# Optimization experiments

Measured on AMD Instinct MI355X. Metric: run time of the kernel, lower is better.

## Reference

```python
import jax, jax.numpy as jnp
import numpy as np

N_HEADS = 16
DIM = 1024
BS, SLEN = 2, 2048
EPS = 1e-12  # F.normalize eps


def setup_inputs() -> dict:
    key = jax.random.key(0)
    ks = jax.random.split(key, 10)
    d = DIM
    inp = {
        "x": jax.random.normal(ks[0], (BS, SLEN, d), dtype=jnp.float32),
        # causal attention mask, as produced by get_masks(causal=True)
        "mask": jnp.tril(jnp.ones((SLEN, SLEN), dtype=bool))[None].repeat(BS, axis=0),
        "Wq": jax.random.normal(ks[1], (d, d), dtype=jnp.float32) / np.sqrt(d),
        "bq": jax.random.normal(ks[2], (d,), dtype=jnp.float32) * 0.02,
        "Wk": jax.random.normal(ks[3], (d, d), dtype=jnp.float32) / np.sqrt(d),
        "bk": jax.random.normal(ks[4], (d,), dtype=jnp.float32) * 0.02,
        "Wv": jax.random.normal(ks[5], (d, d), dtype=jnp.float32) / np.sqrt(d),
        "bv": jax.random.normal(ks[6], (d,), dtype=jnp.float32) * 0.02,
        "Wo": jax.random.normal(ks[7], (d, d), dtype=jnp.float32) / np.sqrt(d),
        "bo": jax.random.normal(ks[8], (d,), dtype=jnp.float32) * 0.02,
        # learnable scale for normalized (cosine) attention
        "attention_scale": jnp.ones((1,), dtype=jnp.float32) / np.sqrt(d // N_HEADS),
    }
    return inp


def _shape(t, bs, h, dph):
    # (bs, len, dim) -> (bs, h, len, dph)
    return t.reshape(bs, -1, h, dph).transpose(0, 2, 1, 3)


def reference(x, mask, Wq, bq, Wk, bk, Wv, bv, Wo, bo, attention_scale):
    bs, qlen, dim = x.shape
    h = N_HEADS
    dph = dim // h

    q = _shape(x @ Wq + bq, bs, h, dph)  # (bs, h, qlen, dph)
    k = _shape(x @ Wk + bk, bs, h, dph)
    v = _shape(x @ Wv + bv, bs, h, dph)

    # normalized (cosine) attention: L2-normalize q and k, learned scale
    q = q / jnp.maximum(jnp.linalg.norm(q, axis=-1, keepdims=True), EPS)
    k = k / jnp.maximum(jnp.linalg.norm(k, axis=-1, keepdims=True), EPS)
    q = q * attention_scale

    scores = jnp.einsum("bhqd,bhkd->bhqk", q, k)  # (bs, h, qlen, klen)
    scores = jnp.where(mask[:, None, :, :], scores, -jnp.inf)
    weights = jax.nn.softmax(scores, axis=-1)

    ctx = jnp.einsum("bhqk,bhkd->bhqd", weights, v)
    ctx = ctx.transpose(0, 2, 1, 3).reshape(bs, qlen, dim)
    return ctx @ Wo + bo
```

## Files before the change

kernel.cpp:

```cpp
#include <hip/hip_runtime.h>
#include <math.h>

#define NH 16
#define DPH 64
#define SLEN 2048
#define BSZ 2
#define DIM 1024
#define NTOK (BSZ * SLEN)
#define LOG2E 1.44269504088896f

typedef unsigned short ushortT;
typedef __attribute__((ext_vector_type(8))) short short8;
typedef __attribute__((ext_vector_type(4))) short s16x4;
typedef __attribute__((ext_vector_type(4))) float f32x4;

typedef __attribute__((address_space(1))) const unsigned int gu32c;
typedef __attribute__((address_space(3))) unsigned int lu32;

__device__ __forceinline__ void gld16(const void* g, void* l) {
    __builtin_amdgcn_global_load_lds((gu32c*)g, (lu32*)l, 16, 0, 0);
}

__device__ __forceinline__ ushortT f2bf(float f) {
    unsigned int u = __builtin_bit_cast(unsigned int, f);
    u = u + 0x7fffu + ((u >> 16) & 1u);
    return (ushortT)(u >> 16);
}

__global__ __launch_bounds__(256) void cvt_all(const float* __restrict__ x,
                                               ushortT* __restrict__ xb,
                                               const float* __restrict__ W0, const float* __restrict__ W1,
                                               const float* __restrict__ W2, const float* __restrict__ W3,
                                               ushortT* __restrict__ T0, ushortT* __restrict__ T1,
                                               ushortT* __restrict__ T2, ushortT* __restrict__ T3) {
    __shared__ float tile[64][65];
    const int tid = threadIdx.x;
    const int bid = blockIdx.x;
    if (bid < 2048) {
        size_t i = (size_t)bid * 256 + tid;
        float4 a = *(const float4*)&x[i * 8];
        float4 b = *(const float4*)&x[i * 8 + 4];
        short8 v;
        v[0] = (short)f2bf(a.x); v[1] = (short)f2bf(a.y);
        v[2] = (short)f2bf(a.z); v[3] = (short)f2bf(a.w);
        v[4] = (short)f2bf(b.x); v[5] = (short)f2bf(b.y);
        v[6] = (short)f2bf(b.z); v[7] = (short)f2bf(b.w);
        *(short8*)&xb[i * 8] = v;
        return;
    }
    const int widx = bid - 2048;
    const int z = widx >> 8, rem = widx & 255;
    const float* W = z == 0 ? W0 : z == 1 ? W1 : z == 2 ? W2 : W3;
    ushortT* T = z == 0 ? T0 : z == 1 ? T1 : z == 2 ? T2 : T3;
    const int kb = (rem >> 4) * 64, nb = (rem & 15) * 64;
#pragma unroll
    for (int it = 0; it < 4; it++) {
        int chunk = it * 256 + tid;
        int r = chunk >> 4, c4 = (chunk & 15) * 4;
        *(float4*)&tile[r][c4] = *(const float4*)&W[(size_t)(kb + r) * DIM + nb + c4];
    }
    __syncthreads();
#pragma unroll
    for (int it = 0; it < 2; it++) {
        int chunk = it * 256 + tid;
        int n = chunk >> 3, k8 = (chunk & 7) * 8;
        short8 o;
#pragma unroll
        for (int j = 0; j < 8; j++) o[j] = (short)f2bf(tile[k8 + j][n]);
        *(short8*)&T[(size_t)(nb + n) * DIM + kb + k8] = o;
    }
}

__global__ __launch_bounds__(512, 2) void gemm_qkv8(const ushortT* __restrict__ A,
                                                    const ushortT* __restrict__ Bt,
                                                    const float* __restrict__ bq,
                                                    const float* __restrict__ bk,
                                                    const float* __restrict__ bv,
                                                    const float* __restrict__ ascale,
                                                    ushortT* __restrict__ Qb,
                                                    ushortT* __restrict__ Kb,
                                                    ushortT* __restrict__ VF) {
    __shared__ __align__(16) ushortT lds[65536];
    const int tid = threadIdx.x;
    const int lane = tid & 63, wid = tid >> 6;
    const int wm = wid >> 2, wn = wid & 3;
    const int lo = lane & 15, hi = lane >> 4;
    const int bid = blockIdx.x;
    const int swz = (bid & 7) * 24 + (bid >> 3);
    const int bx = swz % 12, by = swz / 12;
    const int row0 = by * 256, col0 = bx * 256;
    const int srow2 = tid >> 2, sc = tid & 3;
    f32x4 acc[8][4] = {};
    short8 af[4], bfr[4];

    auto stage = [&](int isA, int buf, int ksh, int kt) {
        const ushortT* g = isA ? A : Bt;
        int r0 = isA ? row0 : col0;
        int base = (isA ? 0 : 32768) + (buf * 2 + ksh) * 8192;
#pragma unroll
        for (int r = 0; r < 2; r++) {
            int rl = r * 128 + srow2;
            int gch = sc ^ ((rl >> 1) & 3);
            gld16(&g[(size_t)(r0 + rl) * DIM + kt * 64 + ksh * 32 + gch * 8],
                  &lds[base + r * 4096 + tid * 8]);
        }
    };
    auto loadA = [&](int buf, int ks, int mh) {
        int base = (buf * 2 + ks) * 8192;
#pragma unroll
        for (int mm = 0; mm < 4; mm++) {
            int row = wm * 128 + (mh * 4 + mm) * 16 + lo;
            af[mm] = *(const short8*)&lds[base + row * 32 + (hi ^ ((row >> 1) & 3)) * 8];
        }
    };
    auto loadB = [&](int buf, int ks) {
        int base = 32768 + (buf * 2 + ks) * 8192;
#pragma unroll
        for (int n = 0; n < 4; n++) {
            int row = wn * 64 + n * 16 + lo;
            bfr[n] = *(const short8*)&lds[base + row * 32 + (hi ^ ((row >> 1) & 3)) * 8];
        }
    };
    auto mfma16 = [&](int mh) {
        __builtin_amdgcn_s_setprio(1);
#pragma unroll
        for (int mm = 0; mm < 4; mm++)
#pragma unroll
            for (int n = 0; n < 4; n++)
                acc[mh * 4 + mm][n] = __builtin_amdgcn_mfma_f32_16x16x32_bf16(
                    af[mm], bfr[n], acc[mh * 4 + mm][n], 0, 0, 0);
        __builtin_amdgcn_s_setprio(0);
    };

    stage(1, 0, 0, 0); stage(0, 0, 0, 0);
    stage(1, 0, 1, 0); stage(0, 0, 1, 0);
    stage(1, 1, 0, 1); stage(0, 1, 0, 1);

#pragma unroll 1
    for (int it = 0; it < 8; ++it) {
        const int o = it * 2 + 1;
        const bool more = (it < 7);
        asm volatile("s_waitcnt vmcnt(8)" ::: "memory");
        asm volatile("s_barrier" ::: "memory");
        loadA(0, 0, 0); loadB(0, 0);
        stage(1, 1, 1, o);
        mfma16(0);
        asm volatile("s_barrier" ::: "memory");
        loadA(0, 0, 1);
        stage(0, 1, 1, o);
        mfma16(1);
        asm volatile("s_waitcnt vmcnt(8)" ::: "memory");
        asm volatile("s_barrier" ::: "memory");
        loadA(0, 1, 0); loadB(0, 1);
        if (more) stage(1, 0, 0, o + 1);
        mfma16(0);
        asm volatile("s_barrier" ::: "memory");
        loadA(0, 1, 1);
        if (more) stage(0, 0, 0, o + 1);
        mfma16(1);
        if (more) { asm volatile("s_waitcnt vmcnt(8)" ::: "memory"); }
        else      { asm volatile("s_waitcnt vmcnt(4)" ::: "memory"); }
        asm volatile("s_barrier" ::: "memory");
        loadA(1, 0, 0); loadB(1, 0);
        if (more) stage(1, 0, 1, o + 1);
        mfma16(0);
        asm volatile("s_barrier" ::: "memory");
        loadA(1, 0, 1);
        if (more) stage(0, 0, 1, o + 1);
        mfma16(1);
        if (more) { asm volatile("s_waitcnt vmcnt(8)" ::: "memory"); }
        else      { asm volatile("s_waitcnt vmcnt(0)" ::: "memory"); }
        asm volatile("s_barrier" ::: "memory");
        loadA(1, 1, 0); loadB(1, 1);
        if (more) stage(1, 1, 0, o + 2);
        mfma16(0);
        asm volatile("s_barrier" ::: "memory");
        loadA(1, 1, 1);
        if (more) stage(0, 1, 0, o + 2);
        mfma16(1);
    }
    __syncthreads();

    const int cg = col0 + wn * 64;
    const int which = cg >> 10;
    const int cwin = cg & 1023;
    const int h = cwin >> 6;
    const int t0g = row0 + wm * 128;
    const int b = t0g >> 11, tok0 = t0g & (SLEN - 1);
    const float* bias = which == 0 ? bq : which == 1 ? bk : bv;

    float bb4[4];
#pragma unroll
    for (int n = 0; n < 4; n++) bb4[n] = bias[cwin + n * 16 + lo];
#pragma unroll
    for (int m = 0; m < 8; m++)
#pragma unroll
        for (int n = 0; n < 4; n++)
#pragma unroll
            for (int r = 0; r < 4; r++) acc[m][n][r] += bb4[n];

    if (which < 2) {
        float asc = (which == 0) ? ascale[0] * LOG2E : 1.0f;
#pragma unroll
        for (int m = 0; m < 8; m++)
#pragma unroll
            for (int r = 0; r < 4; r++) {
                float ss = acc[m][0][r] * acc[m][0][r] + acc[m][1][r] * acc[m][1][r] +
                           acc[m][2][r] * acc[m][2][r] + acc[m][3][r] * acc[m][3][r];
#pragma unroll
                for (int o = 8; o > 0; o >>= 1) ss += __shfl_xor(ss, o);
                float sc2 = asc / fmaxf(sqrtf(ss), 1e-12f);
#pragma unroll
                for (int n = 0; n < 4; n++) acc[m][n][r] *= sc2;
            }
    }

    ushortT* tl = &lds[wid * 8192];
    if (which < 2) {
#pragma unroll
        for (int m = 0; m < 8; m++)
#pragma unroll
            for (int n = 0; n < 4; n++)
#pragma unroll
                for (int r = 0; r < 4; r++) {
                    int row = m * 16 + 4 * hi + r;
                    int c = n * 2 + (lo >> 3);
                    tl[row * 64 + ((c ^ (row & 7)) << 3) + (lo & 7)] = f2bf(acc[m][n][r]);
                }
        ushortT* op = which == 0 ? Qb : Kb;
        const size_t base = ((size_t)(b * NH + h) * SLEN + tok0) * DPH;
#pragma unroll
        for (int j = 0; j < 16; j++) {
            int cid = j * 64 + lane;
            int rowL = cid >> 3, c = cid & 7;
            uint4 v = *(const uint4*)&tl[rowL * 64 + ((c ^ (rowL & 7)) << 3)];
            *(uint4*)&op[base + (size_t)cid * 8] = v;
        }
    } else {
#pragma unroll
        for (int m = 0; m < 8; m++)
#pragma unroll
            for (int n = 0; n < 4; n++)
#pragma unroll
                for (int r = 0; r < 4; r++) {
                    int row = m * 16 + 4 * hi + r;
                    int c = n * 2 + (lo >> 3);
                    tl[row * 64 + ((c ^ ((row >> 3) & 7)) << 3) + (lo & 7)] = f2bf(acc[m][n][r]);
                }
        const int bh = b * NH + h;
        const int kt0 = tok0 >> 6;
#pragma unroll
        for (int i = 0; i < 16; i++) {
            int kk = i >> 3;
            int c = i & 7;
            int jd = c >> 1, ks2 = c & 1;
            int colL = jd * 16 + lo;
            int c2 = colL >> 3;
            short8 v;
#pragma unroll
            for (int e = 0; e < 8; e++) {
                int rowL = kk * 64 + ks2 * 32 + 8 * hi + e;
                v[e] = (short)tl[rowL * 64 + ((c2 ^ ((rowL >> 3) & 7)) << 3) + (colL & 7)];
            }
            *(short8*)&VF[((size_t)bh * 32 + kt0 + kk) * 4096 + (size_t)(c * 64 + lane) * 8] = v;
        }
    }
}

__global__ __launch_bounds__(256) void gemm_oproj(const ushortT* __restrict__ A,
                                                  const ushortT* __restrict__ Bt,
                                                  const float* __restrict__ bias,
                                                  float* __restrict__ outF) {
    __shared__ __align__(16) ushortT lds[32768];
    const int tid = threadIdx.x;
    const int lane = tid & 63, wid = tid >> 6;
    const int wr = wid >> 1, wc = wid & 1;
    const int lo = lane & 15, hi = lane >> 4;
    const int bid = blockIdx.x;
    const int swz = (bid & 7) * 32 + (bid >> 3);
    const int bx = swz & 7, by = swz >> 3;
    const int row0 = by * 128, col0 = bx * 128;
    f32x4 acc[4][4] = {};
    short8 afO[4], bfO[4];

    auto stageO = [&](int isA, int slot, int kh) {
        const ushortT* g = isA ? A : Bt;
        int r0 = isA ? row0 : col0;
        int base = (isA ? 0 : 16384) + slot * 4096;
#pragma unroll
        for (int r = 0; r < 2; r++) {
            int ch = r * 256 + tid;
            int row = ch >> 2, kc = ch & 3;
            gld16(&g[(size_t)(r0 + row) * DIM + kh * 32 + (kc ^ ((row >> 1) & 3)) * 8],
                  &lds[base + r * 2048 + tid * 8]);
        }
    };
    auto loadAO = [&](int slot) {
        int base = slot * 4096;
#pragma unroll
        for (int m = 0; m < 4; m++) {
            int row = wr * 64 + m * 16 + lo;
            afO[m] = *(const short8*)&lds[base + row * 32 + (hi ^ ((row >> 1) & 3)) * 8];
        }
    };
    auto loadBO = [&](int slot) {
        int base = 16384 + slot * 4096;
#pragma unroll
        for (int n = 0; n < 4; n++) {
            int row = wc * 64 + n * 16 + lo;
            bfO[n] = *(const short8*)&lds[base + row * 32 + (hi ^ ((row >> 1) & 3)) * 8];
        }
    };
    auto mfmaO = [&]() {
        __builtin_amdgcn_s_setprio(1);
#pragma unroll
        for (int m = 0; m < 4; m++)
#pragma unroll
            for (int n = 0; n < 4; n++)
                acc[m][n] = __builtin_amdgcn_mfma_f32_16x16x32_bf16(afO[m], bfO[n], acc[m][n], 0, 0, 0);
        __builtin_amdgcn_s_setprio(0);
    };

    stageO(0, 0, 0); stageO(1, 0, 0);
    stageO(0, 1, 1); stageO(1, 1, 1);
    stageO(0, 2, 2); stageO(1, 2, 2);
    asm volatile("s_waitcnt vmcnt(8)" ::: "memory");
    asm volatile("s_barrier" ::: "memory");

#pragma unroll 1
    for (int it = 0; it < 8; ++it) {
        const int k0 = it * 4;
        const bool last = (it == 7);
        loadAO(0); loadBO(0);
        stageO(0, 3, k0 + 3); stageO(1, 3, k0 + 3);
        asm volatile("s_barrier" ::: "memory");
        mfmaO();
        asm volatile("s_waitcnt vmcnt(8)" ::: "memory");
        asm volatile("s_barrier" ::: "memory");
        loadAO(1); loadBO(1);
        if (!last) { stageO(0, 0, k0 + 4); stageO(1, 0, k0 + 4); }
        asm volatile("s_barrier" ::: "memory");
        mfmaO();
        if (!last) { asm volatile("s_waitcnt vmcnt(8)" ::: "memory"); }
        else       { asm volatile("s_waitcnt vmcnt(4)" ::: "memory"); }
        asm volatile("s_barrier" ::: "memory");
        loadAO(2); loadBO(2);
        if (!last) { stageO(0, 1, k0 + 5); stageO(1, 1, k0 + 5); }
        asm volatile("s_barrier" ::: "memory");
        mfmaO();
        if (!last) { asm volatile("s_waitcnt vmcnt(8)" ::: "memory"); }
        else       { asm volatile("s_waitcnt vmcnt(0)" ::: "memory"); }
        asm volatile("s_barrier" ::: "memory");
        loadAO(3); loadBO(3);
        if (!last) { stageO(0, 2, k0 + 6); stageO(1, 2, k0 + 6); }
        asm volatile("s_barrier" ::: "memory");
        mfmaO();
        if (!last) { asm volatile("s_waitcnt vmcnt(8)" ::: "memory"); }
        asm volatile("s_barrier" ::: "memory");
    }
    __syncthreads();

    float bb[4];
#pragma unroll
    for (int n = 0; n < 4; n++) bb[n] = bias[col0 + wc * 64 + n * 16 + lo];
#pragma unroll
    for (int m = 0; m < 4; m++)
#pragma unroll
        for (int n = 0; n < 4; n++)
#pragma unroll
            for (int r = 0; r < 4; r++) acc[m][n][r] += bb[n];

    float* tl = (float*)lds + wid * 4096;
#pragma unroll
    for (int m = 0; m < 4; m++)
#pragma unroll
        for (int n = 0; n < 4; n++)
#pragma unroll
            for (int r = 0; r < 4; r++) {
                int row = m * 16 + hi * 4 + r;
                int col = n * 16 + lo;
                int cc = col >> 2;
                tl[row * 64 + ((cc ^ (row & 7)) << 2) + (col & 3)] = acc[m][n][r];
            }
#pragma unroll
    for (int j = 0; j < 16; j++) {
        int cid = j * 64 + lane;
        int rowR = cid >> 4, cc = cid & 15;
        f32x4 v = *(const f32x4*)&tl[rowR * 64 + ((cc ^ (rowR & 7)) << 2)];
        int rg = row0 + wr * 64 + rowR;
        int cgl = col0 + wc * 64 + cc * 4;
        *(f32x4*)&outF[(size_t)rg * DIM + cgl] = v;
    }
}

__global__ __launch_bounds__(512, 4) void attn(const ushortT* __restrict__ Q,
                                               const ushortT* __restrict__ K,
                                               const ushortT* __restrict__ VF,
                                               const float* __restrict__ scale,
                                               ushortT* __restrict__ ctx) {
    __shared__ __align__(16) ushortT Ks[64 * 64];
    __shared__ __align__(16) ushortT Ps[8 * 16 * 64];
    const int tid = threadIdx.x, lane = tid & 63, wid = tid >> 6;
    const int wg = wid & 3, sg = wid >> 2;
    const int bh = blockIdx.x, p = blockIdx.y;
    const int qt = sg ? p : 31 - p;
    const int kbmax = 31 - p;
    const size_t hb = (size_t)bh * SLEN * DPH;
    const int lo = lane & 15, hi = lane >> 4;
    const float mshift = fabsf(scale[0]) * LOG2E;

    short8 aq[2];
    {
        const int qrow = qt * 64 + wg * 16 + lo;
#pragma unroll
        for (int ks = 0; ks < 2; ks++)
            aq[ks] = *(const short8*)&Q[hb + (size_t)qrow * DPH + ks * 32 + 8 * hi];
    }

    const int srow = tid >> 3, sslot = tid & 7;
    const int sldsoff = srow * 64 + ((sslot ^ (srow & 7)) << 3);
    uint4 kr = *(const uint4*)&K[hb + (size_t)srow * DPH + sslot * 8];
    *(uint4*)&Ks[sldsoff] = kr;
    __syncthreads();

    f32x4 accd[4] = {};
    float lp = 0.f;

    for (int kb = 0; kb <= kbmax; kb++) {
        if (kb < kbmax)
            kr = *(const uint4*)&K[hb + (size_t)((kb + 1) * 64 + srow) * DPH + sslot * 8];

        if (kb <= qt) {
            short8 bv[8];
            const ushortT* vt = &VF[(((size_t)bh * 32 + kb) * 512 + lane) * 8];
#pragma unroll
            for (int c = 0; c < 8; c++) bv[c] = *(const short8*)&vt[(size_t)c * 512];

            f32x4 sf[4] = {};
#pragma unroll
            for (int ks = 0; ks < 2; ks++)
#pragma unroll
                for (int j = 0; j < 4; j++) {
                    int row = j * 16 + lo;
                    short8 bk = *(const short8*)&Ks[row * 64 + (((ks * 4 + hi) ^ (row & 7)) << 3)];
                    sf[j] = __builtin_amdgcn_mfma_f32_16x16x32_bf16(bk, aq[ks], sf[j], 0, 0, 0);
                }

            if (kb == qt) {
#pragma unroll
                for (int j = 0; j < 4; j++)
#pragma unroll
                    for (int r = 0; r < 4; r++)
                        if (j * 16 + 4 * hi + r > wg * 16 + lo) sf[j][r] = -INFINITY;
            }

#pragma unroll
            for (int j = 0; j < 4; j++) {
                s16x4 pk;
#pragma unroll
                for (int r = 0; r < 4; r++) {
                    float pv = __builtin_amdgcn_exp2f(sf[j][r] - mshift);
                    lp += pv;
                    pk[r] = (short)f2bf(pv);
                }
                int slot = (4 * j + hi) ^ (2 * (lo & 7));
                *(s16x4*)&Ps[wid * 1024 + lo * 64 + slot * 4] = pk;
            }

#pragma unroll
            for (int ks = 0; ks < 2; ks++) {
                int slot0 = (8 * ks + 2 * hi) ^ (2 * (lo & 7));
                short8 ap = *(const short8*)&Ps[wid * 1024 + lo * 64 + slot0 * 4];
#pragma unroll
                for (int jd = 0; jd < 4; jd++)
                    accd[jd] = __builtin_amdgcn_mfma_f32_16x16x32_bf16(ap, bv[jd * 2 + ks], accd[jd], 0, 0, 0);
            }
        }

        __syncthreads();
        if (kb < kbmax) {
            *(uint4*)&Ks[sldsoff] = kr;
            __syncthreads();
        }
    }

    lp += __shfl_xor(lp, 16);
    lp += __shfl_xor(lp, 32);

    const int b = bh >> 4, h = bh & 15;
#pragma unroll
    for (int r = 0; r < 4; r++) {
        float lr = __shfl(lp, (lane & 48) | (4 * hi + r));
        float inv = 1.0f / lr;
        int t = qt * 64 + wg * 16 + 4 * hi + r;
#pragma unroll
        for (int jd = 0; jd < 4; jd++) {
            int d = jd * 16 + lo;
            ctx[(size_t)(b * SLEN + t) * DIM + h * 64 + d] = f2bf(accd[jd][r] * inv);
        }
    }
}

extern "C" void kernel_launch(void* const* d_in, const int* in_sizes, int n_in,
                              void* d_out, int out_size, void* d_ws,
                              size_t ws_size, hipStream_t stream) {
    const float* x = (const float*)d_in[0];
    const float* Wq = (const float*)d_in[2];
    const float* bq = (const float*)d_in[3];
    const float* Wk = (const float*)d_in[4];
    const float* bk = (const float*)d_in[5];
    const float* Wv = (const float*)d_in[6];
    const float* bv = (const float*)d_in[7];
    const float* Wo = (const float*)d_in[8];
    const float* bo = (const float*)d_in[9];
    const float* ascale = (const float*)d_in[10];
    float* outF = (float*)d_out;

    unsigned char* ws = (unsigned char*)d_ws;
    const size_t MB = 1u << 20;
    ushortT* xb = (ushortT*)(ws);
    ushortT* Wqkvt = (ushortT*)(ws + 8 * MB);
    ushortT* Wot = (ushortT*)(ws + 14 * MB);
    ushortT* Qb = (ushortT*)(ws + 16 * MB);
    ushortT* Kb = (ushortT*)(ws + 24 * MB);
    ushortT* VFb = (ushortT*)(ws + 32 * MB);
    ushortT* ctxb = (ushortT*)(ws + 40 * MB);

    cvt_all<<<3072, 256, 0, stream>>>(x, xb, Wq, Wk, Wv, Wo, Wqkvt,
                                      Wqkvt + (size_t)1024 * 1024,
                                      Wqkvt + (size_t)2048 * 1024, Wot);

    gemm_qkv8<<<dim3(192), 512, 0, stream>>>(xb, Wqkvt, bq, bk, bv, ascale, Qb, Kb, VFb);

    attn<<<dim3(32, 16), 512, 0, stream>>>(Qb, Kb, VFb, ascale, ctxb);

    gemm_oproj<<<dim3(256), 256, 0, stream>>>(ctxb, Wot, bo, outF);
}
```

Before: 98.49 us.

## Double-buffer attention K tile, use packed bf16 convert, and restructure oproj GEMM to 8 waves

The attention kernel now double-buffers the K tile in LDS, which removes one barrier per key block. It also converts probabilities to bf16 with the packed v_cvt_pk_bf16_f32 instruction instead of software rounding, and raises wave priority around the MFMA sections. The output-projection GEMM moves from 256 to 512 threads with a 2x4 wave layout, a 64-wide k-step and a finer-grained interleave of loads and MFMAs. The aim is to cut sync stalls and VALU cost. In exchange, LDS use grows, rounding changes slightly, and the GEMM's register footprint and schedule shift.

Result: faster. 94.25 us (-4.3%).

```diff
diff --git a/kernel.cpp b/kernel.cpp
--- a/kernel.cpp
+++ b/kernel.cpp
@@ -25,6 +25,12 @@
     unsigned int u = __builtin_bit_cast(unsigned int, f);
     u = u + 0x7fffu + ((u >> 16) & 1u);
     return (ushortT)(u >> 16);
+}
+
+__device__ __forceinline__ unsigned int cvtpk_bf16(float a, float b) {
+    unsigned int r;
+    asm("v_cvt_pk_bf16_f32 %0, %1, %2" : "=v"(r) : "v"(a), "v"(b));
+    return r;
 }
 
 __global__ __launch_bounds__(256) void cvt_all(const float* __restrict__ x,
@@ -267,128 +273,136 @@
     }
 }
 
-__global__ __launch_bounds__(256) void gemm_oproj(const ushortT* __restrict__ A,
-                                                  const ushortT* __restrict__ Bt,
-                                                  const float* __restrict__ bias,
-                                                  float* __restrict__ outF) {
+__global__ __launch_bounds__(512, 2) void gemm_oproj(const ushortT* __restrict__ A,
+                                                     const ushortT* __restrict__ Bt,
+                                                     const float* __restrict__ bias,
+                                                     float* __restrict__ outF) {
     __shared__ __align__(16) ushortT lds[32768];
     const int tid = threadIdx.x;
     const int lane = tid & 63, wid = tid >> 6;
-    const int wr = wid >> 1, wc = wid & 1;
+    const int wm = wid >> 2, wn = wid & 3;
     const int lo = lane & 15, hi = lane >> 4;
     const int bid = blockIdx.x;
     const int swz = (bid & 7) * 32 + (bid >> 3);
     const int bx = swz & 7, by = swz >> 3;
     const int row0 = by * 128, col0 = bx * 128;
-    f32x4 acc[4][4] = {};
-    short8 afO[4], bfO[4];
-
-    auto stageO = [&](int isA, int slot, int kh) {
+    const int srow = tid >> 2, sc = tid & 3;
+    f32x4 acc[4][2] = {};
+    short8 afO[2], bfO[2];
+
+    auto stage = [&](int isA, int buf, int ksh, int kt) {
         const ushortT* g = isA ? A : Bt;
         int r0 = isA ? row0 : col0;
-        int base = (isA ? 0 : 16384) + slot * 4096;
-#pragma unroll
-        for (int r = 0; r < 2; r++) {
-            int ch = r * 256 + tid;
-            int row = ch >> 2, kc = ch & 3;
-            gld16(&g[(size_t)(r0 + row) * DIM + kh * 32 + (kc ^ ((row >> 1) & 3)) * 8],
-                  &lds[base + r * 2048 + tid * 8]);
-        }
-    };
-    auto loadAO = [&](int slot) {
-        int base = slot * 4096;
-#pragma unroll
-        for (int m = 0; m < 4; m++) {
-            int row = wr * 64 + m * 16 + lo;
-            afO[m] = *(const short8*)&lds[base + row * 32 + (hi ^ ((row >> 1) & 3)) * 8];
-        }
-    };
-    auto loadBO = [&](int slot) {
-        int base = 16384 + slot * 4096;
-#pragma unroll
-        for (int n = 0; n < 4; n++) {
-            int row = wc * 64 + n * 16 + lo;
+        int base = (isA ? 0 : 16384) + (buf * 2 + ksh) * 4096;
+        int gch = sc ^ ((srow >> 1) & 3);
+        gld16(&g[(size_t)(r0 + srow) * DIM + kt * 64 + ksh * 32 + gch * 8],
+              &lds[base + tid * 8]);
+    };
+    auto loadAO = [&](int buf, int ks, int mh) {
+        int base = (buf * 2 + ks) * 4096;
+#pragma unroll
+        for (int mm = 0; mm < 2; mm++) {
+            int row = wm * 64 + (mh * 2 + mm) * 16 + lo;
+            afO[mm] = *(const short8*)&lds[base + row * 32 + (hi ^ ((row >> 1) & 3)) * 8];
+        }
+    };
+    auto loadBO = [&](int buf, int ks) {
+        int base = 16384 + (buf * 2 + ks) * 4096;
+#pragma unroll
+        for (int n = 0; n < 2; n++) {
+            int row = wn * 32 + n * 16 + lo;
             bfO[n] = *(const short8*)&lds[base + row * 32 + (hi ^ ((row >> 1) & 3)) * 8];
         }
     };
-    auto mfmaO = [&]() {
+    auto mfma4 = [&](int mh) {
         __builtin_amdgcn_s_setprio(1);
 #pragma unroll
-        for (int m = 0; m < 4; m++)
-#pragma unroll
-            for (int n = 0; n < 4; n++)
-                acc[m][n] = __builtin_amdgcn_mfma_f32_16x16x32_bf16(afO[m], bfO[n], acc[m][n], 0, 0, 0);
+        for (int mm = 0; mm < 2; mm++)
+#pragma unroll
+            for (int n = 0; n < 2; n++)
+                acc[mh * 2 + mm][n] = __builtin_amdgcn_mfma_f32_16x16x32_bf16(
+                    afO[mm], bfO[n], acc[mh * 2 + mm][n], 0, 0, 0);
         __builtin_amdgcn_s_setprio(0);
     };
 
-    stageO(0, 0, 0); stageO(1, 0, 0);
-    stageO(0, 1, 1); stageO(1, 1, 1);
-    stageO(0, 2, 2); stageO(1, 2, 2);
-    asm volatile("s_waitcnt vmcnt(8)" ::: "memory");
-    asm volatile("s_barrier" ::: "memory");
+    stage(1, 0, 0, 0); stage(0, 0, 0, 0);
+    stage(1, 0, 1, 0); stage(0, 0, 1, 0);
+    stage(1, 1, 0, 1); stage(0, 1, 0, 1);
 
 #pragma unroll 1
     for (int it = 0; it < 8; ++it) {
-        const int k0 = it * 4;
-        const bool last = (it == 7);
-        loadAO(0); loadBO(0);
-        stageO(0, 3, k0 + 3); stageO(1, 3, k0 + 3);
-        asm volatile("s_barrier" ::: "memory");
-        mfmaO();
-        asm volatile("s_waitcnt vmcnt(8)" ::: "memory");
-        asm volatile("s_barrier" ::: "memory");
-        loadAO(1); loadBO(1);
-        if (!last) { stageO(0, 0, k0 + 4); stageO(1, 0, k0 + 4); }
-        asm volatile("s_barrier" ::: "memory");
-        mfmaO();
-        if (!last) { asm volatile("s_waitcnt vmcnt(8)" ::: "memory"); }
-        else       { asm volatile("s_waitcnt vmcnt(4)" ::: "memory"); }
-        asm volatile("s_barrier" ::: "memory");
-        loadAO(2); loadBO(2);
-        if (!last) { stageO(0, 1, k0 + 5); stageO(1, 1, k0 + 5); }
-        asm volatile("s_barrier" ::: "memory");
-        mfmaO();
-        if (!last) { asm volatile("s_waitcnt vmcnt(8)" ::: "memory"); }
-        else       { asm volatile("s_waitcnt vmcnt(0)" ::: "memory"); }
-        asm volatile("s_barrier" ::: "memory");
-        loadAO(3); loadBO(3);
-        if (!last) { stageO(0, 2, k0 + 6); stageO(1, 2, k0 + 6); }
-        asm volatile("s_barrier" ::: "memory");
-        mfmaO();
-        if (!last) { asm volatile("s_waitcnt vmcnt(8)" ::: "memory"); }
-        asm volatile("s_barrier" ::: "memory");
+        const int o = it * 2 + 1;
+        const bool more = (it < 7);
+        asm volatile("s_waitcnt vmcnt(4)" ::: "memory");
+        asm volatile("s_barrier" ::: "memory");
+        loadAO(0, 0, 0); loadBO(0, 0);
+        stage(1, 1, 1, o);
+        mfma4(0);
+        asm volatile("s_barrier" ::: "memory");
+        loadAO(0, 0, 1);
+        stage(0, 1, 1, o);
+        mfma4(1);
+        asm volatile("s_waitcnt vmcnt(4)" ::: "memory");
+        asm volatile("s_barrier" ::: "memory");
+        loadAO(0, 1, 0); loadBO(0, 1);
+        if (more) stage(1, 0, 0, o + 1);
+        mfma4(0);
+        asm volatile("s_barrier" ::: "memory");
+        loadAO(0, 1, 1);
+        if (more) stage(0, 0, 0, o + 1);
+        mfma4(1);
+        if (more) { asm volatile("s_waitcnt vmcnt(4)" ::: "memory"); }
+        else      { asm volatile("s_waitcnt vmcnt(2)" ::: "memory"); }
+        asm volatile("s_barrier" ::: "memory");
+        loadAO(1, 0, 0); loadBO(1, 0);
+        if (more) stage(1, 0, 1, o + 1);
+        mfma4(0);
+        asm volatile("s_barrier" ::: "memory");
+        loadAO(1, 0, 1);
+        if (more) stage(0, 0, 1, o + 1);
+        mfma4(1);
+        if (more) { asm volatile("s_waitcnt vmcnt(4)" ::: "memory"); }
+        else      { asm volatile("s_waitcnt vmcnt(0)" ::: "memory"); }
+        asm volatile("s_barrier" ::: "memory");
+        loadAO(1, 1, 0); loadBO(1, 1);
+        if (more) stage(1, 1, 0, o + 2);
+        mfma4(0);
+        asm volatile("s_barrier" ::: "memory");
+        loadAO(1, 1, 1);
+        if (more) stage(0, 1, 0, o + 2);
+        mfma4(1);
     }
     __syncthreads();
 
-    float bb[4];
-#pragma unroll
-    for (int n = 0; n < 4; n++) bb[n] = bias[col0 + wc * 64 + n * 16 + lo];
+    float bb[2];
+#pragma unroll
+    for (int n = 0; n < 2; n++) bb[n] = bias[col0 + wn * 32 + n * 16 + lo];
 #pragma unroll
     for (int m = 0; m < 4; m++)
 #pragma unroll
-        for (int n = 0; n < 4; n++)
+        for (int n = 0; n < 2; n++)
 #pragma unroll
             for (int r = 0; r < 4; r++) acc[m][n][r] += bb[n];
 
-    float* tl = (float*)lds + wid * 4096;
+    float* tl = (float*)&lds[wid * 4096];
 #pragma unroll
     for (int m = 0; m < 4; m++)
 #pragma unroll
-        for (int n = 0; n < 4; n++)
+        for (int n = 0; n < 2; n++)
 #pragma unroll
             for (int r = 0; r < 4; r++) {
                 int row = m * 16 + hi * 4 + r;
                 int col = n * 16 + lo;
                 int cc = col >> 2;
-                tl[row * 64 + ((cc ^ (row & 7)) << 2) + (col & 3)] = acc[m][n][r];
+                tl[row * 32 + ((cc ^ (row & 7)) << 2) + (col & 3)] = acc[m][n][r];
             }
 #pragma unroll
-    for (int j = 0; j < 16; j++) {
+    for (int j = 0; j < 8; j++) {
         int cid = j * 64 + lane;
-        int rowR = cid >> 4, cc = cid & 15;
-        f32x4 v = *(const f32x4*)&tl[rowR * 64 + ((cc ^ (rowR & 7)) << 2)];
-        int rg = row0 + wr * 64 + rowR;
-        int cgl = col0 + wc * 64 + cc * 4;
+        int rowR = cid >> 3, cc = cid & 7;
+        f32x4 v = *(const f32x4*)&tl[rowR * 32 + ((cc ^ (rowR & 7)) << 2)];
+        int rg = row0 + wm * 64 + rowR;
+        int cgl = col0 + wn * 32 + cc * 4;
         *(f32x4*)&outF[(size_t)rg * DIM + cgl] = v;
     }
 }
@@ -398,7 +412,7 @@
                                                const ushortT* __restrict__ VF,
                                                const float* __restrict__ scale,
                                                ushortT* __restrict__ ctx) {
-    __shared__ __align__(16) ushortT Ks[64 * 64];
+    __shared__ __align__(16) ushortT Ks[2][64 * 64];
     __shared__ __align__(16) ushortT Ps[8 * 16 * 64];
     const int tid = threadIdx.x, lane = tid & 63, wid = tid >> 6;
     const int wg = wid & 3, sg = wid >> 2;
@@ -420,13 +434,14 @@
     const int srow = tid >> 3, sslot = tid & 7;
     const int sldsoff = srow * 64 + ((sslot ^ (srow & 7)) << 3);
     uint4 kr = *(const uint4*)&K[hb + (size_t)srow * DPH + sslot * 8];
-    *(uint4*)&Ks[sldsoff] = kr;
+    *(uint4*)&Ks[0][sldsoff] = kr;
     __syncthreads();
 
     f32x4 accd[4] = {};
     float lp = 0.f;
 
     for (int kb = 0; kb <= kbmax; kb++) {
+        const int cur = kb & 1;
         if (kb < kbmax)
             kr = *(const uint4*)&K[hb + (size_t)((kb + 1) * 64 + srow) * DPH + sslot * 8];
 
@@ -437,14 +452,16 @@
             for (int c = 0; c < 8; c++) bv[c] = *(const short8*)&vt[(size_t)c * 512];
 
             f32x4 sf[4] = {};
+            __builtin_amdgcn_s_setprio(1);
 #pragma unroll
             for (int ks = 0; ks < 2; ks++)
 #pragma unroll
                 for (int j = 0; j < 4; j++) {
                     int row = j * 16 + lo;
-                    short8 bk = *(const short8*)&Ks[row * 64 + (((ks * 4 + hi) ^ (row & 7)) << 3)];
+                    short8 bk = *(const short8*)&Ks[cur][row * 64 + (((ks * 4 + hi) ^ (row & 7)) << 3)];
                     sf[j] = __builtin_amdgcn_mfma_f32_16x16x32_bf16(bk, aq[ks], sf[j], 0, 0, 0);
                 }
+            __builtin_amdgcn_s_setprio(0);
 
             if (kb == qt) {
 #pragma unroll
@@ -456,17 +473,19 @@
 
 #pragma unroll
             for (int j = 0; j < 4; j++) {
-                s16x4 pk;
-#pragma unroll
-                for (int r = 0; r < 4; r++) {
-                    float pv = __builtin_amdgcn_exp2f(sf[j][r] - mshift);
-                    lp += pv;
-                    pk[r] = (short)f2bf(pv);
-                }
+                float pv0 = __builtin_amdgcn_exp2f(sf[j][0] - mshift);
+                float pv1 = __builtin_amdgcn_exp2f(sf[j][1] - mshift);
+                float pv2 = __builtin_amdgcn_exp2f(sf[j][2] - mshift);
+                float pv3 = __builtin_amdgcn_exp2f(sf[j][3] - mshift);
+                lp += (pv0 + pv1) + (pv2 + pv3);
+                uint2 pk;
+                pk.x = cvtpk_bf16(pv0, pv1);
+                pk.y = cvtpk_bf16(pv2, pv3);
                 int slot = (4 * j + hi) ^ (2 * (lo & 7));
-                *(s16x4*)&Ps[wid * 1024 + lo * 64 + slot * 4] = pk;
+                *(uint2*)&Ps[wid * 1024 + lo * 64 + slot * 4] = pk;
             }
 
+            __builtin_amdgcn_s_setprio(1);
 #pragma unroll
             for (int ks = 0; ks < 2; ks++) {
                 int slot0 = (8 * ks + 2 * hi) ^ (2 * (lo & 7));
@@ -475,13 +494,11 @@
                 for (int jd = 0; jd < 4; jd++)
                     accd[jd] = __builtin_amdgcn_mfma_f32_16x16x32_bf16(ap, bv[jd * 2 + ks], accd[jd], 0, 0, 0);
             }
-        }
-
+            __builtin_amdgcn_s_setprio(0);
+        }
+
+        if (kb < kbmax) *(uint4*)&Ks[cur ^ 1][sldsoff] = kr;
         __syncthreads();
-        if (kb < kbmax) {
-            *(uint4*)&Ks[sldsoff] = kr;
-            __syncthreads();
-        }
     }
 
     lp += __shfl_xor(lp, 16);
@@ -534,5 +551,5 @@
 
     attn<<<dim3(32, 16), 512, 0, stream>>>(Qb, Kb, VFb, ascale, ctxb);
 
-    gemm_oproj<<<dim3(256), 256, 0, stream>>>(ctxb, Wot, bo, outF);
-}
+    gemm_oproj<<<dim3(256), 512, 0, stream>>>(ctxb, Wot, bo, outF);
+}
```
